# Performance work log

Measured on AMD Instinct MI355X. Metric: run time of the kernel, lower is better.

The kernel has to match this reference:

```python
import jax, jax.numpy as jnp
import numpy as np

B, L, E, D1, D2 = 256, 128, 64, 512, 512


def setup_inputs() -> dict:
    key = jax.random.key(0)
    k1, k2, k3, kw = jax.random.split(key, 4)
    tensor1 = jax.random.normal(k1, (B, L, D1), dtype=jnp.float32)
    tensor2 = jax.random.normal(k2, (B, L, D2), dtype=jnp.float32)
    parameters_index = jax.random.randint(k3, (B,), 0, E, dtype=jnp.int32)
    # xavier_uniform with relu gain: gain*sqrt(6/(fan_in+fan_out)),
    # torch fan for [E,D1,D2]: fan_in = D1*D2, fan_out = E*D2
    gain = float(np.sqrt(2.0))
    bound = gain * float(np.sqrt(6.0 / (D1 * D2 + E * D2)))
    weights = jax.random.uniform(kw, (E, D1, D2), minval=-bound, maxval=bound, dtype=jnp.float32)
    return {"tensor1": tensor1, "tensor2": tensor2, "parameters_index": parameters_index, "weights": weights}


def reference(tensor1, tensor2, parameters_index, weights):
    # gather per-batch weight matrix [B, D1, D2], then bilinear form x1^T W x2
    w = weights[parameters_index]  # [B, D1, D2]
    # equals: sum over i,j of tensor1[b,l,i] * w[b,i,j] * tensor2[b,l,j] -> [B, L]
    return jnp.einsum('bli,bij,blj->bl', tensor1, w, tensor2)
```

## Files before the change

### kernel.cpp

```cpp
#include <hip/hip_runtime.h>
#include <stdint.h>

#define NB 256
#define NL 128
#define ND1 512
#define ND2 512
#define NE 64

#define BI 128
#define BK 64
#define NKT (ND2 / BK)
#define LDST 72
#define BUFSZ ((NL + BI) * LDST)

typedef float float4_t __attribute__((ext_vector_type(4)));
typedef __bf16 bf16x8_t __attribute__((ext_vector_type(8)));
typedef unsigned short ushort4_t __attribute__((ext_vector_type(4)));
typedef unsigned short ushort8_t __attribute__((ext_vector_type(8)));

__device__ __forceinline__ unsigned short f2bf(float f) {
    unsigned int u = __float_as_uint(f);
    u += 0x7FFFu + ((u >> 16) & 1u);
    return (unsigned short)(u >> 16);
}

__device__ __forceinline__ ushort4_t cvt4(float4_t v) {
    ushort4_t u;
    u.x = f2bf(v.x); u.y = f2bf(v.y); u.z = f2bf(v.z); u.w = f2bf(v.w);
    return u;
}

__global__ void pre_kernel(const int* __restrict__ pidx, int* __restrict__ perm,
                           float* __restrict__ out, int zero_n, int do_sort)
{
    const int g = blockIdx.x, t = threadIdx.x;
    const int idx = g * 256 + t;
    if (idx < zero_n) out[idx] = 0.f;
    if (do_sort && g == 0) {
        __shared__ int cnt[NE];
        __shared__ int base[NE];
        if (t < NE) cnt[t] = 0;
        __syncthreads();
        const int e = pidx[t];
        const int r = atomicAdd(&cnt[e], 1);
        __syncthreads();
        if (t == 0) {
            int s = 0;
            for (int i = 0; i < NE; ++i) { base[i] = s; s += cnt[i]; }
        }
        __syncthreads();
        perm[base[e] + r] = t;
    }
}

template <bool USE_PERM>
__global__ __launch_bounds__(512, 4) void pdot_kernel(
    const float* __restrict__ t1, const float* __restrict__ t2,
    const int* __restrict__ pidx, const float* __restrict__ wgt,
    const int* __restrict__ perm, float* __restrict__ out)
{
    __shared__ unsigned short sm[2][BUFSZ];

    const int g  = blockIdx.x;
    const int x  = g & 7;
    const int s  = g >> 3;
    const int slot = x * 32 + (s >> 2);
    const int b  = USE_PERM ? perm[slot] : slot;
    const int it = s & 3;
    const int i0 = it * BI;

    const int t  = threadIdx.x;
    const int w  = t >> 6;
    const int wv = w & 3;
    const int ih = w >> 2;
    const int ln = t & 63;
    const int nh = ln & 15;
    const int qd = ln >> 4;

    const int e = pidx[b];
    const float* aPtr = t2  + (size_t)b * (NL * ND2);
    const float* bPtr = wgt + (size_t)e * (ND1 * ND2) + (size_t)i0 * ND2;
    const float* t1p  = t1  + (size_t)b * (NL * ND1) + i0 + ih * 64;

    float4_t acc[2][4];
    #pragma unroll
    for (int i = 0; i < 2; ++i)
        #pragma unroll
        for (int j = 0; j < 4; ++j) {
            float4_t z = {0.f, 0.f, 0.f, 0.f};
            acc[i][j] = z;
        }

    const int s_row = t >> 4;
    const int s_kq  = (t & 15) * 4;
    const size_t sOff = (size_t)s_row * ND2 + s_kq;
    const int wOffA = s_row * LDST + s_kq;
    const int wOffB = (NL + s_row) * LDST + s_kq;

    float4_t pa[4], pb[4];

    #pragma unroll
    for (int p = 0; p < 4; ++p) {
        pa[p] = *(const float4_t*)(aPtr + sOff + (size_t)p * (32 * ND2));
        pb[p] = *(const float4_t*)(bPtr + sOff + (size_t)p * (32 * ND2));
    }
    #pragma unroll
    for (int p = 0; p < 4; ++p) {
        *(ushort4_t*)(&sm[0][wOffA + p * (32 * LDST)]) = cvt4(pa[p]);
        *(ushort4_t*)(&sm[0][wOffB + p * (32 * LDST)]) = cvt4(pb[p]);
    }
    #pragma unroll
    for (int p = 0; p < 4; ++p) {
        pa[p] = *(const float4_t*)(aPtr + sOff + BK + (size_t)p * (32 * ND2));
        pb[p] = *(const float4_t*)(bPtr + sOff + BK + (size_t)p * (32 * ND2));
    }
    __builtin_amdgcn_sched_barrier(0);
    asm volatile("s_waitcnt lgkmcnt(0)" ::: "memory");
    __builtin_amdgcn_sched_barrier(0);
    __builtin_amdgcn_s_barrier();
    __builtin_amdgcn_sched_barrier(0);

    #pragma unroll
    for (int kt = 0; kt < NKT; ++kt) {
        const int cur = kt & 1;
        const int nxt = cur ^ 1;
        const unsigned short* cA = &sm[cur][0];
        const unsigned short* cB = &sm[cur][NL * LDST];

        if (kt < NKT - 1) {
            #pragma unroll
            for (int p = 0; p < 4; ++p) {
                *(ushort4_t*)(&sm[nxt][wOffA + p * (32 * LDST)]) = cvt4(pa[p]);
                *(ushort4_t*)(&sm[nxt][wOffB + p * (32 * LDST)]) = cvt4(pb[p]);
            }
            if (kt < NKT - 2) {
                const size_t k0 = (size_t)(kt + 2) * BK;
                #pragma unroll
                for (int p = 0; p < 4; ++p) {
                    pa[p] = *(const float4_t*)(aPtr + sOff + k0 + (size_t)p * (32 * ND2));
                    pb[p] = *(const float4_t*)(bPtr + sOff + k0 + (size_t)p * (32 * ND2));
                }
                __builtin_amdgcn_sched_barrier(0);
            }
        }

        #pragma unroll
        for (int ks = 0; ks < 2; ++ks) {
            const int kf = ks * 32 + qd * 8;
            const int ra = wv * 32 + nh;
            bf16x8_t af0 = __builtin_bit_cast(bf16x8_t, *(const ushort8_t*)(&cA[(ra     ) * LDST + kf]));
            bf16x8_t af1 = __builtin_bit_cast(bf16x8_t, *(const ushort8_t*)(&cA[(ra + 16) * LDST + kf]));
            bf16x8_t bv[4];
            #pragma unroll
            for (int ns = 0; ns < 4; ++ns)
                bv[ns] = __builtin_bit_cast(bf16x8_t, *(const ushort8_t*)(&cB[(ih * 64 + ns * 16 + nh) * LDST + kf]));
            __builtin_amdgcn_s_setprio(1);
            #pragma unroll
            for (int ns = 0; ns < 4; ++ns) {
                acc[0][ns] = __builtin_amdgcn_mfma_f32_16x16x32_bf16(af0, bv[ns], acc[0][ns], 0, 0, 0);
                acc[1][ns] = __builtin_amdgcn_mfma_f32_16x16x32_bf16(af1, bv[ns], acc[1][ns], 0, 0, 0);
            }
            __builtin_amdgcn_s_setprio(0);
        }

        if (kt < NKT - 1) {
            asm volatile("s_waitcnt lgkmcnt(0)" ::: "memory");
            __builtin_amdgcn_sched_barrier(0);
            __builtin_amdgcn_s_barrier();
            __builtin_amdgcn_sched_barrier(0);
        }
    }

    #pragma unroll
    for (int ms = 0; ms < 2; ++ms) {
        #pragma unroll
        for (int r = 0; r < 4; ++r) {
            const int row = wv * 32 + ms * 16 + qd * 4 + r;
            float ps = 0.f;
            #pragma unroll
            for (int ns = 0; ns < 4; ++ns) {
                const float tv = t1p[(size_t)row * ND1 + ns * 16 + nh];
                ps += acc[ms][ns][r] * tv;
            }
            ps += __shfl_xor(ps, 1);
            ps += __shfl_xor(ps, 2);
            ps += __shfl_xor(ps, 4);
            ps += __shfl_xor(ps, 8);
            if (nh == 0) atomicAdd(&out[b * NL + row], ps);
        }
    }
}

extern "C" void kernel_launch(void* const* d_in, const int* in_sizes, int n_in,
                              void* d_out, int out_size, void* d_ws, size_t ws_size,
                              hipStream_t stream)
{
    const float* t1  = (const float*)d_in[0];
    const float* t2  = (const float*)d_in[1];
    const int* pidx  = (const int*)d_in[2];
    const float* wgt = (const float*)d_in[3];
    float* out = (float*)d_out;

    const int zero_blocks = (out_size + 255) / 256;
    const bool have_ws = ws_size >= NB * sizeof(int);
    int* perm = have_ws ? (int*)d_ws : nullptr;

    pre_kernel<<<dim3(zero_blocks), dim3(256), 0, stream>>>(pidx, perm, out, out_size, have_ws ? 1 : 0);

    if (have_ws)
        pdot_kernel<true><<<dim3(NB * (ND1 / BI)), dim3(512), 0, stream>>>(t1, t2, pidx, wgt, perm, out);
    else
        pdot_kernel<false><<<dim3(NB * (ND1 / BI)), dim3(512), 0, stream>>>(t1, t2, pidx, wgt, nullptr, out);
}
```

Before: 207.8 us.

## Stream fp32 tiles directly to LDS via global_load_lds and convert at fragment read

Replaces the register-staged global load, bf16 convert and LDS store pipeline with direct global-to-LDS 16-byte loads of fp32 data into an XOR-swizzled single buffer. Fragments are read as fp32 from LDS and converted to bf16 just before the MFMAs. This removes VGPR staging and the store instructions, but doubles LDS footprint per tile, drops double buffering so loads now block between k-steps, and lowers the occupancy hint to 2.

Measured after the change: 216.6 us. 4.2% more time.

```diff
diff --git a/kernel.cpp b/kernel.cpp
--- a/kernel.cpp
+++ b/kernel.cpp
@@ -10,24 +10,19 @@
 #define BI 128
 #define BK 64
 #define NKT (ND2 / BK)
-#define LDST 72
-#define BUFSZ ((NL + BI) * LDST)
 
 typedef float float4_t __attribute__((ext_vector_type(4)));
 typedef __bf16 bf16x8_t __attribute__((ext_vector_type(8)));
-typedef unsigned short ushort4_t __attribute__((ext_vector_type(4)));
-typedef unsigned short ushort8_t __attribute__((ext_vector_type(8)));
-
-__device__ __forceinline__ unsigned short f2bf(float f) {
-    unsigned int u = __float_as_uint(f);
-    u += 0x7FFFu + ((u >> 16) & 1u);
-    return (unsigned short)(u >> 16);
-}
-
-__device__ __forceinline__ ushort4_t cvt4(float4_t v) {
-    ushort4_t u;
-    u.x = f2bf(v.x); u.y = f2bf(v.y); u.z = f2bf(v.z); u.w = f2bf(v.w);
-    return u;
+
+#define GLOAD16(gp, lp) __builtin_amdgcn_global_load_lds( \
+    (const __attribute__((address_space(1))) void*)(gp),  \
+    (__attribute__((address_space(3))) void*)(lp), 16, 0, 0)
+
+__device__ __forceinline__ bf16x8_t cvt8f(float4_t lo, float4_t hi) {
+    bf16x8_t r;
+    r[0] = (__bf16)lo.x; r[1] = (__bf16)lo.y; r[2] = (__bf16)lo.z; r[3] = (__bf16)lo.w;
+    r[4] = (__bf16)hi.x; r[5] = (__bf16)hi.y; r[6] = (__bf16)hi.z; r[7] = (__bf16)hi.w;
+    return r;
 }
 
 __global__ void pre_kernel(const int* __restrict__ pidx, int* __restrict__ perm,
@@ -54,12 +49,12 @@
 }
 
 template <bool USE_PERM>
-__global__ __launch_bounds__(512, 4) void pdot_kernel(
+__global__ __launch_bounds__(512, 2) void pdot_kernel(
     const float* __restrict__ t1, const float* __restrict__ t2,
     const int* __restrict__ pidx, const float* __restrict__ wgt,
     const int* __restrict__ perm, float* __restrict__ out)
 {
-    __shared__ unsigned short sm[2][BUFSZ];
+    __shared__ float sm[2 * NL * BK];
 
     const int g  = blockIdx.x;
     const int x  = g & 7;
@@ -91,80 +86,77 @@
             acc[i][j] = z;
         }
 
-    const int s_row = t >> 4;
-    const int s_kq  = (t & 15) * 4;
-    const size_t sOff = (size_t)s_row * ND2 + s_kq;
-    const int wOffA = s_row * LDST + s_kq;
-    const int wOffB = (NL + s_row) * LDST + s_kq;
-
-    float4_t pa[4], pb[4];
-
-    #pragma unroll
-    for (int p = 0; p < 4; ++p) {
-        pa[p] = *(const float4_t*)(aPtr + sOff + (size_t)p * (32 * ND2));
-        pb[p] = *(const float4_t*)(bPtr + sOff + (size_t)p * (32 * ND2));
-    }
-    #pragma unroll
-    for (int p = 0; p < 4; ++p) {
-        *(ushort4_t*)(&sm[0][wOffA + p * (32 * LDST)]) = cvt4(pa[p]);
-        *(ushort4_t*)(&sm[0][wOffB + p * (32 * LDST)]) = cvt4(pb[p]);
-    }
-    #pragma unroll
-    for (int p = 0; p < 4; ++p) {
-        pa[p] = *(const float4_t*)(aPtr + sOff + BK + (size_t)p * (32 * ND2));
-        pb[p] = *(const float4_t*)(bPtr + sOff + BK + (size_t)p * (32 * ND2));
+    const float* aSrc[4];
+    const float* bSrc[4];
+    unsigned dstByte[4];
+    #pragma unroll
+    for (int q = 0; q < 4; ++q) {
+        const int sl = w * 256 + q * 64 + ln;
+        const int r  = sl >> 4;
+        const int c  = sl & 15;
+        const int m  = (r >> 1) & 7;
+        const int cr = c ^ m;
+        const int off = r * ND2 + cr * 4;
+        aSrc[q] = aPtr + off;
+        bSrc[q] = bPtr + off;
+        dstByte[q] = (unsigned)((w * 256 + q * 64) * 16);
+    }
+    char* const smB = (char*)&sm[0];
+
+    const int m  = (nh >> 1) & 7;
+    const int cs = ((qd * 2) ^ m) << 4;
+    const int raA = wv * 32 + nh;
+    const int aRow0 = raA * 256;
+    const int bRowBase = (ih * 64 + nh) * 256;
+
+    #pragma unroll
+    for (int q = 0; q < 4; ++q) {
+        GLOAD16(aSrc[q], smB + dstByte[q]);
+        GLOAD16(bSrc[q], smB + 32768 + dstByte[q]);
     }
     __builtin_amdgcn_sched_barrier(0);
-    asm volatile("s_waitcnt lgkmcnt(0)" ::: "memory");
+    asm volatile("s_waitcnt vmcnt(0)" ::: "memory");
     __builtin_amdgcn_sched_barrier(0);
     __builtin_amdgcn_s_barrier();
     __builtin_amdgcn_sched_barrier(0);
 
-    #pragma unroll
     for (int kt = 0; kt < NKT; ++kt) {
-        const int cur = kt & 1;
-        const int nxt = cur ^ 1;
-        const unsigned short* cA = &sm[cur][0];
-        const unsigned short* cB = &sm[cur][NL * LDST];
-
-        if (kt < NKT - 1) {
-            #pragma unroll
-            for (int p = 0; p < 4; ++p) {
-                *(ushort4_t*)(&sm[nxt][wOffA + p * (32 * LDST)]) = cvt4(pa[p]);
-                *(ushort4_t*)(&sm[nxt][wOffB + p * (32 * LDST)]) = cvt4(pb[p]);
-            }
-            if (kt < NKT - 2) {
-                const size_t k0 = (size_t)(kt + 2) * BK;
-                #pragma unroll
-                for (int p = 0; p < 4; ++p) {
-                    pa[p] = *(const float4_t*)(aPtr + sOff + k0 + (size_t)p * (32 * ND2));
-                    pb[p] = *(const float4_t*)(bPtr + sOff + k0 + (size_t)p * (32 * ND2));
-                }
-                __builtin_amdgcn_sched_barrier(0);
-            }
-        }
-
         #pragma unroll
         for (int ks = 0; ks < 2; ++ks) {
-            const int kf = ks * 32 + qd * 8;
-            const int ra = wv * 32 + nh;
-            bf16x8_t af0 = __builtin_bit_cast(bf16x8_t, *(const ushort8_t*)(&cA[(ra     ) * LDST + kf]));
-            bf16x8_t af1 = __builtin_bit_cast(bf16x8_t, *(const ushort8_t*)(&cA[(ra + 16) * LDST + kf]));
-            bf16x8_t bv[4];
-            #pragma unroll
-            for (int ns = 0; ns < 4; ++ns)
-                bv[ns] = __builtin_bit_cast(bf16x8_t, *(const ushort8_t*)(&cB[(ih * 64 + ns * 16 + nh) * LDST + kf]));
-            __builtin_amdgcn_s_setprio(1);
+            const int cb = cs + ks * 128;
+            float4_t lo0 = *(const float4_t*)(smB + (aRow0        + cb));
+            float4_t hi0 = *(const float4_t*)(smB + ((aRow0       + cb) ^ 16));
+            float4_t lo1 = *(const float4_t*)(smB + (aRow0 + 4096 + cb));
+            float4_t hi1 = *(const float4_t*)(smB + ((aRow0 + 4096 + cb) ^ 16));
+            bf16x8_t af0 = cvt8f(lo0, hi0);
+            bf16x8_t af1 = cvt8f(lo1, hi1);
             #pragma unroll
             for (int ns = 0; ns < 4; ++ns) {
-                acc[0][ns] = __builtin_amdgcn_mfma_f32_16x16x32_bf16(af0, bv[ns], acc[0][ns], 0, 0, 0);
-                acc[1][ns] = __builtin_amdgcn_mfma_f32_16x16x32_bf16(af1, bv[ns], acc[1][ns], 0, 0, 0);
+                const int ba = 32768 + bRowBase + ns * 4096 + cb;
+                float4_t bl = *(const float4_t*)(smB + ba);
+                float4_t bh = *(const float4_t*)(smB + (ba ^ 16));
+                bf16x8_t bv = cvt8f(bl, bh);
+                __builtin_amdgcn_s_setprio(1);
+                acc[0][ns] = __builtin_amdgcn_mfma_f32_16x16x32_bf16(af0, bv, acc[0][ns], 0, 0, 0);
+                acc[1][ns] = __builtin_amdgcn_mfma_f32_16x16x32_bf16(af1, bv, acc[1][ns], 0, 0, 0);
+                __builtin_amdgcn_s_setprio(0);
             }
-            __builtin_amdgcn_s_setprio(0);
         }
 
         if (kt < NKT - 1) {
+            __builtin_amdgcn_sched_barrier(0);
             asm volatile("s_waitcnt lgkmcnt(0)" ::: "memory");
+            __builtin_amdgcn_sched_barrier(0);
+            __builtin_amdgcn_s_barrier();
+            __builtin_amdgcn_sched_barrier(0);
+            const int fo = (kt + 1) * BK;
+            #pragma unroll
+            for (int q = 0; q < 4; ++q) {
+                GLOAD16(aSrc[q] + fo, smB + dstByte[q]);
+                GLOAD16(bSrc[q] + fo, smB + 32768 + dstByte[q]);
+            }
+            __builtin_amdgcn_sched_barrier(0);
+            asm volatile("s_waitcnt vmcnt(0)" ::: "memory");
             __builtin_amdgcn_sched_barrier(0);
             __builtin_amdgcn_s_barrier();
             __builtin_amdgcn_sched_barrier(0);
```
